# Performance work log

Measured on AMD Instinct MI355X. Metric: run time of the kernel, lower is better.

## Reference

```python
import jax, jax.numpy as jnp
import numpy as np

EPS = 1e-12

def setup_inputs() -> dict:
    key = jax.random.key(0)
    k1, k2, k3, k4 = jax.random.split(key, 4)
    N_TABLE, N_NODES, N_SAMP, D_IN, D_OUT = 200000, 50000, 32, 256, 256
    features = jax.random.normal(k1, (N_TABLE, D_IN), dtype=jnp.float32)
    node_idx = jax.random.randint(k2, (N_NODES,), 0, N_TABLE)
    neigh_idx = jax.random.randint(k3, (N_NODES, N_SAMP), 0, N_TABLE)
    W = jax.random.normal(k4, (D_IN, D_OUT), dtype=jnp.float32) / np.sqrt(D_IN)
    b = jnp.zeros((D_OUT,), dtype=jnp.float32)
    return {"node_idx": node_idx, "neigh_idx": neigh_idx, "features": features, "W": W, "b": b}

def reference(node_idx, neigh_idx, features, W, b):
    # MeanAggregator with self_loop: mean over sampled neighbors + the node itself
    n_samp = neigh_idx.shape[1]
    neigh_feats = features[neigh_idx]            # [N, S, D] gather
    self_feats = features[node_idx]              # [N, D]
    agg = (neigh_feats.sum(axis=1) + self_feats) / (n_samp + 1)  # [N, D]
    # Combine: linear -> ReLU activation -> L2 normalize
    out = jax.nn.relu(agg @ W + b)               # [N, D_out]
    norm = jnp.sqrt(jnp.sum(out * out, axis=-1, keepdims=True))
    out = out / jnp.maximum(norm, EPS)
    return out
```

## Files before the change

### kernel.cpp

```cpp
#include <hip/hip_runtime.h>
#include <hip/hip_bf16.h>

typedef __attribute__((ext_vector_type(8))) short short8;
typedef __attribute__((ext_vector_type(4))) float f32x4;

#define D_IN   256
#define D_OUT  256
#define NSAMP  32

static __device__ __forceinline__ unsigned short f2bf(float f) {
    unsigned int u = __builtin_bit_cast(unsigned int, f);
    u += 0x7fffu + ((u >> 16) & 1u);
    return (unsigned short)(u >> 16);
}

static __device__ __forceinline__ void accum8(float* a, uint4 v) {
    a[0] += __builtin_bit_cast(float, v.x << 16);
    a[1] += __builtin_bit_cast(float, v.x & 0xffff0000u);
    a[2] += __builtin_bit_cast(float, v.y << 16);
    a[3] += __builtin_bit_cast(float, v.y & 0xffff0000u);
    a[4] += __builtin_bit_cast(float, v.z << 16);
    a[5] += __builtin_bit_cast(float, v.z & 0xffff0000u);
    a[6] += __builtin_bit_cast(float, v.w << 16);
    a[7] += __builtin_bit_cast(float, v.w & 0xffff0000u);
}

__global__ void wconv_kernel(const float* __restrict__ W,
                             unsigned short* __restrict__ wsw) {
    const int k = blockIdx.x;
    const int n = threadIdx.x;
    const float v = W[k * D_OUT + n];
    const int ks = k >> 5, kg = (k >> 3) & 3, j = k & 7;
    const int nf = n >> 4, c = n & 15;
    const int lane = kg * 16 + c;
    const int dst = ((ks * 16 + nf) * 64 + lane) * 8 + j;
    wsw[dst] = f2bf(v);
}

__global__ __launch_bounds__(256, 2) void ygemm_kernel(
        const float* __restrict__ feat,
        const unsigned short* __restrict__ wsw,
        unsigned short* __restrict__ Y,
        int n_table)
{
    __shared__ __attribute__((aligned(16))) unsigned char lds[128 * 512];

    const int tid  = threadIdx.x;
    const int wv   = tid >> 6;
    const int lane = tid & 63;
    const int row0 = blockIdx.x * 128;

    #pragma unroll 8
    for (int it = 0; it < 32; ++it) {
        const int idx = it * 256 + tid;
        const int r   = idx >> 6;
        const int c4  = idx & 63;
        const int grow = row0 + r;
        float4 f = make_float4(0.f, 0.f, 0.f, 0.f);
        if (grow < n_table)
            f = *(const float4*)(feat + (size_t)grow * D_IN + c4 * 4);
        ushort4 pk;
        pk.x = f2bf(f.x); pk.y = f2bf(f.y); pk.z = f2bf(f.z); pk.w = f2bf(f.w);
        unsigned int bo = (unsigned int)(r * 512 + c4 * 8) ^ ((unsigned int)(r & 7) << 4);
        *(ushort4*)(&lds[bo]) = pk;
    }
    __syncthreads();

    f32x4 acc[2][16];
    #pragma unroll
    for (int s = 0; s < 2; ++s)
        #pragma unroll
        for (int i = 0; i < 16; ++i) acc[s][i] = (f32x4)(0.0f);

    const int arow0 = wv * 32 + (lane & 15);
    const int acol  = (lane >> 4) * 16;
    const short8* __restrict__ wp = (const short8*)wsw;

    #pragma unroll
    for (int ks = 0; ks < 8; ++ks) {
        unsigned int bo0 = (unsigned int)(arow0 * 512 + ks * 64 + acol)
                         ^ ((unsigned int)(arow0 & 7) << 4);
        unsigned int bo1 = (unsigned int)((arow0 + 16) * 512 + ks * 64 + acol)
                         ^ ((unsigned int)((arow0 + 16) & 7) << 4);
        const short8 af0 = *(const short8*)(&lds[bo0]);
        const short8 af1 = *(const short8*)(&lds[bo1]);
        #pragma unroll
        for (int nf = 0; nf < 16; ++nf) {
            const short8 bfrag = wp[(ks * 16 + nf) * 64 + lane];
            acc[0][nf] = __builtin_amdgcn_mfma_f32_16x16x32_bf16(af0, bfrag, acc[0][nf], 0, 0, 0);
            acc[1][nf] = __builtin_amdgcn_mfma_f32_16x16x32_bf16(af1, bfrag, acc[1][nf], 0, 0, 0);
        }
    }

    const int c0 = lane & 15;
    #pragma unroll
    for (int s = 0; s < 2; ++s) {
        const int rbase = row0 + wv * 32 + s * 16 + (lane >> 4) * 4;
        #pragma unroll
        for (int j = 0; j < 4; ++j) {
            const int rg = rbase + j;
            if (rg < n_table) {
                #pragma unroll
                for (int nf = 0; nf < 16; ++nf)
                    Y[(size_t)rg * D_OUT + nf * 16 + c0] = f2bf(acc[s][nf][j]);
            }
        }
    }
}

__global__ __launch_bounds__(256) void gather_kernel(
        const int*  __restrict__ node_idx,
        const int*  __restrict__ neigh_idx,
        const unsigned short* __restrict__ Y,
        const float* __restrict__ bias,
        float* __restrict__ out,
        int n_nodes)
{
    const int tid  = threadIdx.x;
    const int l    = tid & 31;
    const int node = blockIdx.x * 8 + (tid >> 5);
    const bool valid = node < n_nodes;

    const int nb   = valid ? neigh_idx[node * NSAMP + l] : 0;
    const int sidx = valid ? node_idx[node] : 0;

    float a[8] = {0.f, 0.f, 0.f, 0.f, 0.f, 0.f, 0.f, 0.f};

    #pragma unroll 8
    for (int s = 0; s < NSAMP; ++s) {
        const int idx = __shfl(nb, s, 32);
        const uint4 v = *(const uint4*)(Y + (size_t)idx * D_OUT + l * 8);
        accum8(a, v);
    }
    {
        const uint4 v = *(const uint4*)(Y + (size_t)sidx * D_OUT + l * 8);
        accum8(a, v);
    }

    const float sc = 1.0f / (float)(NSAMP + 1);
    const float4 b0 = *(const float4*)(bias + l * 8);
    const float4 b1 = *(const float4*)(bias + l * 8 + 4);
    float o[8];
    o[0] = fmaxf(a[0] * sc + b0.x, 0.f);
    o[1] = fmaxf(a[1] * sc + b0.y, 0.f);
    o[2] = fmaxf(a[2] * sc + b0.z, 0.f);
    o[3] = fmaxf(a[3] * sc + b0.w, 0.f);
    o[4] = fmaxf(a[4] * sc + b1.x, 0.f);
    o[5] = fmaxf(a[5] * sc + b1.y, 0.f);
    o[6] = fmaxf(a[6] * sc + b1.z, 0.f);
    o[7] = fmaxf(a[7] * sc + b1.w, 0.f);

    float p = 0.f;
    #pragma unroll
    for (int j = 0; j < 8; ++j) p += o[j] * o[j];
    #pragma unroll
    for (int m = 1; m < 32; m <<= 1) p += __shfl_xor(p, m, 64);
    const float inv = 1.0f / fmaxf(sqrtf(p), 1e-12f);

    if (valid) {
        float4 s0, s1;
        s0.x = o[0] * inv; s0.y = o[1] * inv; s0.z = o[2] * inv; s0.w = o[3] * inv;
        s1.x = o[4] * inv; s1.y = o[5] * inv; s1.z = o[6] * inv; s1.w = o[7] * inv;
        float* op = out + (size_t)node * D_OUT + l * 8;
        *(float4*)op       = s0;
        *(float4*)(op + 4) = s1;
    }
}

__global__ __launch_bounds__(256, 4) void gcn_fused_kernel(
        const int*  __restrict__ node_idx,
        const int*  __restrict__ neigh_idx,
        const float* __restrict__ features,
        const unsigned short* __restrict__ wsw,
        const float* __restrict__ bias,
        float* __restrict__ out,
        int n_nodes)
{
    __shared__ __attribute__((aligned(16))) unsigned char lds[64 * D_IN * 2];

    const int tid  = threadIdx.x;
    const int wv   = tid >> 6;
    const int lane = tid & 63;
    const int block_m0 = blockIdx.x * 64;

    const float scale = 1.0f / (float)(NSAMP + 1);
    for (int r = 0; r < 16; ++r) {
        const int row  = wv * 16 + r;
        const int node = block_m0 + row;
        float ax = 0.f, ay = 0.f, az = 0.f, aw = 0.f;
        if (node < n_nodes) {
            const int nb   = neigh_idx[node * NSAMP + (lane & 31)];
            const int self = node_idx[node];
            {
                const float4 v = *(const float4*)(features + (size_t)self * D_IN + lane * 4);
                ax += v.x; ay += v.y; az += v.z; aw += v.w;
            }
            #pragma unroll 8
            for (int s = 0; s < NSAMP; ++s) {
                const int idx = __shfl(nb, s, 64);
                const float4 v = *(const float4*)(features + (size_t)idx * D_IN + lane * 4);
                ax += v.x; ay += v.y; az += v.z; aw += v.w;
            }
            ax *= scale; ay *= scale; az *= scale; aw *= scale;
        }
        ushort4 pk;
        pk.x = f2bf(ax); pk.y = f2bf(ay); pk.z = f2bf(az); pk.w = f2bf(aw);
        unsigned int bo = (unsigned int)(row * 512 + lane * 8) ^ ((unsigned int)(row & 7) << 4);
        *(ushort4*)(&lds[bo]) = pk;
    }
    __syncthreads();

    f32x4 acc[16];
    #pragma unroll
    for (int i = 0; i < 16; ++i) acc[i] = (f32x4)(0.0f);

    const int arow = wv * 16 + (lane & 15);
    const int acol = (lane >> 4) * 16;
    const short8* __restrict__ wp = (const short8*)wsw;

    #pragma unroll
    for (int ks = 0; ks < 8; ++ks) {
        unsigned int bo = (unsigned int)(arow * 512 + ks * 64 + acol)
                        ^ ((unsigned int)(arow & 7) << 4);
        const short8 afrag = *(const short8*)(&lds[bo]);
        #pragma unroll
        for (int nf = 0; nf < 16; ++nf) {
            const short8 bfrag = wp[(ks * 16 + nf) * 64 + lane];
            acc[nf] = __builtin_amdgcn_mfma_f32_16x16x32_bf16(afrag, bfrag, acc[nf], 0, 0, 0);
        }
    }

    float p[4] = {0.f, 0.f, 0.f, 0.f};
    #pragma unroll
    for (int nf = 0; nf < 16; ++nf) {
        const float bv = bias[nf * 16 + (lane & 15)];
        #pragma unroll
        for (int j = 0; j < 4; ++j) {
            float v = acc[nf][j] + bv;
            v = fmaxf(v, 0.0f);
            acc[nf][j] = v;
            p[j] += v * v;
        }
    }
    #pragma unroll
    for (int m = 1; m < 16; m <<= 1) {
        p[0] += __shfl_xor(p[0], m, 64);
        p[1] += __shfl_xor(p[1], m, 64);
        p[2] += __shfl_xor(p[2], m, 64);
        p[3] += __shfl_xor(p[3], m, 64);
    }
    float inv[4];
    #pragma unroll
    for (int j = 0; j < 4; ++j)
        inv[j] = 1.0f / fmaxf(sqrtf(p[j]), 1e-12f);

    const int rbase = block_m0 + wv * 16 + (lane >> 4) * 4;
    const int c0 = lane & 15;
    #pragma unroll
    for (int j = 0; j < 4; ++j) {
        const int rg = rbase + j;
        if (rg < n_nodes) {
            #pragma unroll
            for (int nf = 0; nf < 16; ++nf)
                out[(size_t)rg * D_OUT + nf * 16 + c0] = acc[nf][j] * inv[j];
        }
    }
}

extern "C" void kernel_launch(void* const* d_in, const int* in_sizes, int n_in,
                              void* d_out, int out_size, void* d_ws, size_t ws_size,
                              hipStream_t stream) {
    const int*   node_idx  = (const int*)d_in[0];
    const int*   neigh_idx = (const int*)d_in[1];
    const float* features  = (const float*)d_in[2];
    const float* W         = (const float*)d_in[3];
    const float* bias      = (const float*)d_in[4];
    float*       out       = (float*)d_out;
    const int n_nodes = in_sizes[0];
    const int n_table = in_sizes[2] / D_IN;

    unsigned short* wsw = (unsigned short*)d_ws;
    unsigned short* Y   = (unsigned short*)((char*)d_ws + 131072);

    const size_t need = 131072 + (size_t)n_table * D_OUT * 2;

    hipLaunchKernelGGL(wconv_kernel, dim3(D_IN), dim3(D_OUT), 0, stream, W, wsw);

    if (ws_size >= need) {
        const int yblocks = (n_table + 127) / 128;
        hipLaunchKernelGGL(ygemm_kernel, dim3(yblocks), dim3(256), 0, stream,
                           features, wsw, Y, n_table);
        const int gblocks = (n_nodes + 7) / 8;
        hipLaunchKernelGGL(gather_kernel, dim3(gblocks), dim3(256), 0, stream,
                           node_idx, neigh_idx, Y, bias, out, n_nodes);
    } else {
        const int nblocks = (n_nodes + 63) / 64;
        hipLaunchKernelGGL(gcn_fused_kernel, dim3(nblocks), dim3(256), 0, stream,
                           node_idx, neigh_idx, features, wsw, bias, out, n_nodes);
    }
}
```

Before: 514.9 us.

## Make Y-GEMM persistent with register-resident W and LDS-staged coalesced stores

The precompute GEMM (features @ W over the whole table) becomes a persistent kernel of 512 blocks looping over 64-row tiles. Each wave loads its 64-column slice of bf16 W into registers once, so W fragments are no longer re-read from global memory for every MFMA. Output tiles go through swizzled LDS and are written as 16-byte row-contiguous stores instead of scattered 2-byte stores. The cost is extra barriers per tile, high register pressure from holding 32 W fragments, and no overlap between tile loads and compute.

```diff
diff --git a/kernel.cpp b/kernel.cpp
--- a/kernel.cpp
+++ b/kernel.cpp
@@ -43,68 +43,91 @@
         unsigned short* __restrict__ Y,
         int n_table)
 {
-    __shared__ __attribute__((aligned(16))) unsigned char lds[128 * 512];
+    __shared__ __attribute__((aligned(16))) unsigned char lds[64 * 512];
 
     const int tid  = threadIdx.x;
     const int wv   = tid >> 6;
     const int lane = tid & 63;
-    const int row0 = blockIdx.x * 128;
-
-    #pragma unroll 8
-    for (int it = 0; it < 32; ++it) {
-        const int idx = it * 256 + tid;
-        const int r   = idx >> 6;
-        const int c4  = idx & 63;
-        const int grow = row0 + r;
-        float4 f = make_float4(0.f, 0.f, 0.f, 0.f);
-        if (grow < n_table)
-            f = *(const float4*)(feat + (size_t)grow * D_IN + c4 * 4);
-        ushort4 pk;
-        pk.x = f2bf(f.x); pk.y = f2bf(f.y); pk.z = f2bf(f.z); pk.w = f2bf(f.w);
-        unsigned int bo = (unsigned int)(r * 512 + c4 * 8) ^ ((unsigned int)(r & 7) << 4);
-        *(ushort4*)(&lds[bo]) = pk;
-    }
-    __syncthreads();
-
-    f32x4 acc[2][16];
-    #pragma unroll
-    for (int s = 0; s < 2; ++s)
-        #pragma unroll
-        for (int i = 0; i < 16; ++i) acc[s][i] = (f32x4)(0.0f);
-
-    const int arow0 = wv * 32 + (lane & 15);
-    const int acol  = (lane >> 4) * 16;
+
     const short8* __restrict__ wp = (const short8*)wsw;
-
-    #pragma unroll
-    for (int ks = 0; ks < 8; ++ks) {
-        unsigned int bo0 = (unsigned int)(arow0 * 512 + ks * 64 + acol)
-                         ^ ((unsigned int)(arow0 & 7) << 4);
-        unsigned int bo1 = (unsigned int)((arow0 + 16) * 512 + ks * 64 + acol)
-                         ^ ((unsigned int)((arow0 + 16) & 7) << 4);
-        const short8 af0 = *(const short8*)(&lds[bo0]);
-        const short8 af1 = *(const short8*)(&lds[bo1]);
-        #pragma unroll
-        for (int nf = 0; nf < 16; ++nf) {
-            const short8 bfrag = wp[(ks * 16 + nf) * 64 + lane];
-            acc[0][nf] = __builtin_amdgcn_mfma_f32_16x16x32_bf16(af0, bfrag, acc[0][nf], 0, 0, 0);
-            acc[1][nf] = __builtin_amdgcn_mfma_f32_16x16x32_bf16(af1, bfrag, acc[1][nf], 0, 0, 0);
-        }
-    }
-
-    const int c0 = lane & 15;
-    #pragma unroll
-    for (int s = 0; s < 2; ++s) {
-        const int rbase = row0 + wv * 32 + s * 16 + (lane >> 4) * 4;
-        #pragma unroll
-        for (int j = 0; j < 4; ++j) {
-            const int rg = rbase + j;
-            if (rg < n_table) {
+    short8 breg[8][4];
+    #pragma unroll
+    for (int ks = 0; ks < 8; ++ks)
+        #pragma unroll
+        for (int n = 0; n < 4; ++n)
+            breg[ks][n] = wp[(ks * 16 + wv * 4 + n) * 64 + lane];
+
+    const int ntiles = (n_table + 63) >> 6;
+    for (int t = blockIdx.x; t < ntiles; t += gridDim.x) {
+        const int row0 = t << 6;
+
+        #pragma unroll 8
+        for (int it = 0; it < 16; ++it) {
+            const int idx = it * 256 + tid;
+            const int r   = idx >> 6;
+            const int c4  = idx & 63;
+            const int grow = row0 + r;
+            float4 f = make_float4(0.f, 0.f, 0.f, 0.f);
+            if (grow < n_table)
+                f = *(const float4*)(feat + (size_t)grow * D_IN + c4 * 4);
+            ushort4 pk;
+            pk.x = f2bf(f.x); pk.y = f2bf(f.y); pk.z = f2bf(f.z); pk.w = f2bf(f.w);
+            unsigned int bo = (unsigned int)(r * 512 + c4 * 8) ^ ((unsigned int)(r & 7) << 4);
+            *(ushort4*)(&lds[bo]) = pk;
+        }
+        __syncthreads();
+
+        f32x4 acc[4][4];
+        #pragma unroll
+        for (int r = 0; r < 4; ++r)
+            #pragma unroll
+            for (int n = 0; n < 4; ++n)
+                acc[r][n] = (f32x4)(0.0f);
+
+        const int acol = (lane >> 4) * 16;
+        #pragma unroll
+        for (int ks = 0; ks < 8; ++ks) {
+            #pragma unroll
+            for (int r = 0; r < 4; ++r) {
+                const int arow = r * 16 + (lane & 15);
+                unsigned int bo = (unsigned int)(arow * 512 + ks * 64 + acol)
+                                ^ ((unsigned int)(arow & 7) << 4);
+                const short8 af = *(const short8*)(&lds[bo]);
                 #pragma unroll
-                for (int nf = 0; nf < 16; ++nf)
-                    Y[(size_t)rg * D_OUT + nf * 16 + c0] = f2bf(acc[s][nf][j]);
+                for (int n = 0; n < 4; ++n)
+                    acc[r][n] = __builtin_amdgcn_mfma_f32_16x16x32_bf16(af, breg[ks][n], acc[r][n], 0, 0, 0);
             }
         }
+        __syncthreads();
+
+        #pragma unroll
+        for (int r = 0; r < 4; ++r)
+            #pragma unroll
+            for (int n = 0; n < 4; ++n)
+                #pragma unroll
+                for (int j = 0; j < 4; ++j) {
+                    const int row = r * 16 + (lane >> 4) * 4 + j;
+                    const int col = (wv * 4 + n) * 16 + (lane & 15);
+                    unsigned int bo = (unsigned int)(row * 512 + col * 2)
+                                    ^ ((unsigned int)(row & 7) << 4);
+                    *(unsigned short*)(&lds[bo]) = f2bf(acc[r][n][j]);
+                }
+        __syncthreads();
+
+        const int orow = tid >> 2;
+        const int ochk = (tid & 3) * 128;
+        const int grow = row0 + orow;
+        if (grow < n_table) {
+            char* yrow = (char*)(Y + (size_t)grow * D_OUT);
+            #pragma unroll
+            for (int i = 0; i < 8; ++i) {
+                unsigned int bo = (unsigned int)(orow * 512 + ochk + i * 16)
+                                ^ ((unsigned int)(orow & 7) << 4);
+                const uint4 v = *(const uint4*)(&lds[bo]);
+                *(uint4*)(yrow + ochk + i * 16) = v;
+            }
+        }
+        __syncthreads();
     }
 }
 
@@ -287,8 +310,7 @@
     hipLaunchKernelGGL(wconv_kernel, dim3(D_IN), dim3(D_OUT), 0, stream, W, wsw);
 
     if (ws_size >= need) {
-        const int yblocks = (n_table + 127) / 128;
-        hipLaunchKernelGGL(ygemm_kernel, dim3(yblocks), dim3(256), 0, stream,
+        hipLaunchKernelGGL(ygemm_kernel, dim3(512), dim3(256), 0, stream,
                            features, wsw, Y, n_table);
         const int gblocks = (n_nodes + 7) / 8;
         hipLaunchKernelGGL(gather_kernel, dim3(gblocks), dim3(256), 0, stream,
```

Measured after the change: 633.8 us. 1.23x slower.

## Make Y-GEMM persistent with batched loads and LDS-staged coalesced output

Applied to the files above, without the earlier changes.

The GEMM that projects the whole feature table becomes a persistent kernel: a fixed grid of 512 blocks loops over 128-row tiles. Feature loads are batched as 16 float4s per thread before conversion, giving more loads in flight. The bf16 results are staged through swizzled LDS so each thread writes 16-byte contiguous chunks of Y, replacing scattered 2-byte global stores. The cost is extra LDS traffic and barriers per tile, plus higher register pressure from the load batch.

```diff
diff --git a/kernel.cpp b/kernel.cpp
--- a/kernel.cpp
+++ b/kernel.cpp
@@ -48,63 +48,96 @@
     const int tid  = threadIdx.x;
     const int wv   = tid >> 6;
     const int lane = tid & 63;
-    const int row0 = blockIdx.x * 128;
-
-    #pragma unroll 8
-    for (int it = 0; it < 32; ++it) {
-        const int idx = it * 256 + tid;
-        const int r   = idx >> 6;
-        const int c4  = idx & 63;
-        const int grow = row0 + r;
-        float4 f = make_float4(0.f, 0.f, 0.f, 0.f);
-        if (grow < n_table)
-            f = *(const float4*)(feat + (size_t)grow * D_IN + c4 * 4);
-        ushort4 pk;
-        pk.x = f2bf(f.x); pk.y = f2bf(f.y); pk.z = f2bf(f.z); pk.w = f2bf(f.w);
-        unsigned int bo = (unsigned int)(r * 512 + c4 * 8) ^ ((unsigned int)(r & 7) << 4);
-        *(ushort4*)(&lds[bo]) = pk;
-    }
-    __syncthreads();
-
-    f32x4 acc[2][16];
-    #pragma unroll
-    for (int s = 0; s < 2; ++s)
-        #pragma unroll
-        for (int i = 0; i < 16; ++i) acc[s][i] = (f32x4)(0.0f);
-
-    const int arow0 = wv * 32 + (lane & 15);
-    const int acol  = (lane >> 4) * 16;
     const short8* __restrict__ wp = (const short8*)wsw;
 
-    #pragma unroll
-    for (int ks = 0; ks < 8; ++ks) {
-        unsigned int bo0 = (unsigned int)(arow0 * 512 + ks * 64 + acol)
-                         ^ ((unsigned int)(arow0 & 7) << 4);
-        unsigned int bo1 = (unsigned int)((arow0 + 16) * 512 + ks * 64 + acol)
-                         ^ ((unsigned int)((arow0 + 16) & 7) << 4);
-        const short8 af0 = *(const short8*)(&lds[bo0]);
-        const short8 af1 = *(const short8*)(&lds[bo1]);
-        #pragma unroll
-        for (int nf = 0; nf < 16; ++nf) {
-            const short8 bfrag = wp[(ks * 16 + nf) * 64 + lane];
-            acc[0][nf] = __builtin_amdgcn_mfma_f32_16x16x32_bf16(af0, bfrag, acc[0][nf], 0, 0, 0);
-            acc[1][nf] = __builtin_amdgcn_mfma_f32_16x16x32_bf16(af1, bfrag, acc[1][nf], 0, 0, 0);
-        }
-    }
-
-    const int c0 = lane & 15;
-    #pragma unroll
-    for (int s = 0; s < 2; ++s) {
-        const int rbase = row0 + wv * 32 + s * 16 + (lane >> 4) * 4;
-        #pragma unroll
-        for (int j = 0; j < 4; ++j) {
-            const int rg = rbase + j;
-            if (rg < n_table) {
+    const int ntiles = (n_table + 127) >> 7;
+    for (int t = blockIdx.x; t < ntiles; t += gridDim.x) {
+        const int row0 = t << 7;
+
+        #pragma unroll
+        for (int b = 0; b < 2; ++b) {
+            float4 v[16];
+            #pragma unroll
+            for (int j = 0; j < 8; ++j) {
+                const int P  = b * 2048 + j * 256 + tid;
+                const int r  = P >> 5;
+                const int cp = P & 31;
+                int grow = row0 + r;
+                if (grow > n_table - 1) grow = n_table - 1;
+                const float* src = feat + (size_t)grow * D_IN + cp * 8;
+                v[j * 2]     = *(const float4*)(src);
+                v[j * 2 + 1] = *(const float4*)(src + 4);
+            }
+            #pragma unroll
+            for (int j = 0; j < 8; ++j) {
+                const int P  = b * 2048 + j * 256 + tid;
+                const int r  = P >> 5;
+                const int cp = P & 31;
+                short8 pk;
+                pk[0] = (short)f2bf(v[j*2].x);   pk[1] = (short)f2bf(v[j*2].y);
+                pk[2] = (short)f2bf(v[j*2].z);   pk[3] = (short)f2bf(v[j*2].w);
+                pk[4] = (short)f2bf(v[j*2+1].x); pk[5] = (short)f2bf(v[j*2+1].y);
+                pk[6] = (short)f2bf(v[j*2+1].z); pk[7] = (short)f2bf(v[j*2+1].w);
+                unsigned int bo = (unsigned int)(r * 512 + cp * 16)
+                                ^ ((unsigned int)(r & 7) << 4);
+                *(short8*)(&lds[bo]) = pk;
+            }
+        }
+        __syncthreads();
+
+        f32x4 acc[2][16];
+        #pragma unroll
+        for (int s = 0; s < 2; ++s)
+            #pragma unroll
+            for (int i = 0; i < 16; ++i) acc[s][i] = (f32x4)(0.0f);
+
+        const int arow0 = wv * 32 + (lane & 15);
+        const int acol  = (lane >> 4) * 16;
+        #pragma unroll
+        for (int ks = 0; ks < 8; ++ks) {
+            unsigned int bo0 = (unsigned int)(arow0 * 512 + ks * 64 + acol)
+                             ^ ((unsigned int)(arow0 & 7) << 4);
+            unsigned int bo1 = (unsigned int)((arow0 + 16) * 512 + ks * 64 + acol)
+                             ^ ((unsigned int)((arow0 + 16) & 7) << 4);
+            const short8 af0 = *(const short8*)(&lds[bo0]);
+            const short8 af1 = *(const short8*)(&lds[bo1]);
+            #pragma unroll
+            for (int nf = 0; nf < 16; ++nf) {
+                const short8 bfrag = wp[(ks * 16 + nf) * 64 + lane];
+                acc[0][nf] = __builtin_amdgcn_mfma_f32_16x16x32_bf16(af0, bfrag, acc[0][nf], 0, 0, 0);
+                acc[1][nf] = __builtin_amdgcn_mfma_f32_16x16x32_bf16(af1, bfrag, acc[1][nf], 0, 0, 0);
+            }
+        }
+        __syncthreads();
+
+        #pragma unroll
+        for (int s = 0; s < 2; ++s)
+            #pragma unroll
+            for (int nf = 0; nf < 16; ++nf)
                 #pragma unroll
-                for (int nf = 0; nf < 16; ++nf)
-                    Y[(size_t)rg * D_OUT + nf * 16 + c0] = f2bf(acc[s][nf][j]);
-            }
-        }
+                for (int j = 0; j < 4; ++j) {
+                    const int row = wv * 32 + s * 16 + (lane >> 4) * 4 + j;
+                    const int col = nf * 16 + (lane & 15);
+                    unsigned int bo = (unsigned int)(row * 512 + col * 2)
+                                    ^ ((unsigned int)(row & 7) << 4);
+                    *(unsigned short*)(&lds[bo]) = f2bf(acc[s][nf][j]);
+                }
+        __syncthreads();
+
+        const int orow = tid >> 1;
+        const int ochk = (tid & 1) * 256;
+        const int grow = row0 + orow;
+        if (grow < n_table) {
+            char* yrow = (char*)(Y + (size_t)grow * D_OUT);
+            #pragma unroll
+            for (int i = 0; i < 16; ++i) {
+                unsigned int bo = (unsigned int)(orow * 512 + ochk + i * 16)
+                                ^ ((unsigned int)(orow & 7) << 4);
+                const uint4 v = *(const uint4*)(&lds[bo]);
+                *(uint4*)(yrow + ochk + i * 16) = v;
+            }
+        }
+        __syncthreads();
     }
 }
 
@@ -287,8 +320,7 @@
     hipLaunchKernelGGL(wconv_kernel, dim3(D_IN), dim3(D_OUT), 0, stream, W, wsw);
 
     if (ws_size >= need) {
-        const int yblocks = (n_table + 127) / 128;
-        hipLaunchKernelGGL(ygemm_kernel, dim3(yblocks), dim3(256), 0, stream,
+        hipLaunchKernelGGL(ygemm_kernel, dim3(512), dim3(256), 0, stream,
                            features, wsw, Y, n_table);
         const int gblocks = (n_nodes + 7) / 8;
         hipLaunchKernelGGL(gather_kernel, dim3(gblocks), dim3(256), 0, stream,
```

Measured after the change: 953.6 us. +85.2%, slower.
